# Kernel tuning notes

Measured on AMD Instinct MI355X. Metric: run time of the kernel, lower is better.

Reference implementation:

```python
import jax, jax.numpy as jnp
import numpy as np

N = 25000   # nodes of type 'window'
E = 200000  # edges per relation
H = 512     # hidden_channels
OUT = 250   # out_channels
L = 4       # num_layers
R = 3       # relations: near, close, sim


def setup_inputs() -> dict:
    key = jax.random.key(0)
    ks = jax.random.split(key, 8)
    s = 1.0 / np.sqrt(H).astype(np.float32)
    x = jax.random.normal(ks[0], (N, H), jnp.float32)
    W_pre = jax.random.normal(ks[1], (H, H), jnp.float32) * s
    W_post = jax.random.normal(ks[2], (H, H), jnp.float32) * s
    Wl = jax.random.normal(ks[3], (L, R, H, H), jnp.float32) * s   # SAGEConv lin_l (neighbors)
    Wr = jax.random.normal(ks[4], (L, R, H, H), jnp.float32) * s   # SAGEConv lin_r (root)
    bl = jnp.zeros((L, R, H), jnp.float32)                         # lin_l bias
    W_out = jax.random.normal(ks[5], (H, OUT), jnp.float32) * s
    b_out = jnp.zeros((OUT,), jnp.float32)
    edges = jax.random.randint(ks[6], (R, 2, E), 0, N, jnp.int32)  # [rel, (src,dst), E]
    return dict(x=x, W_pre=W_pre, W_post=W_post, Wl=Wl, Wr=Wr, bl=bl,
                W_out=W_out, b_out=b_out, edges=edges)


def _leaky(v):
    return jnp.where(v >= 0, v, 0.2 * v)


def reference(x, W_pre, W_post, Wl, Wr, bl, W_out, b_out, edges):
    # pretransform + post_transform: leaky(leaky(x @ Wpre) @ Wpost)
    h = _leaky(_leaky(x @ W_pre) @ W_post)

    # per-relation destination in-degree (constant across layers)
    inv_deg = []
    for r in range(R):
        cnt = jax.ops.segment_sum(jnp.ones((E,), h.dtype), edges[r, 1], num_segments=N)
        inv_deg.append(1.0 / jnp.maximum(cnt, 1.0))  # [N]

    for l in range(L):
        acc = jnp.zeros_like(h)
        for r in range(R):
            src, dst = edges[r, 0], edges[r, 1]
            # mean aggregation of neighbor features over destinations
            agg = jax.ops.segment_sum(h[src], dst, num_segments=N) * inv_deg[r][:, None]
            # SAGEConv: lin_l(agg) + lin_r(x_root)
            acc = acc + (agg @ Wl[l, r] + bl[l, r] + h @ Wr[l, r])
        # HeteroConv aggr='mean' across relations, then LeakyReLU(0.2)
        h = _leaky(acc / R)

    return h @ W_out + b_out
```

## Files before the change

kernel.cpp:

```cpp
#include <hip/hip_runtime.h>

#define N_ 25000
#define E_ 200000
#define H_ 512
#define OUT_ 250
#define WSZ (H_ * H_)

typedef unsigned short u16;
typedef unsigned int u32;
typedef __bf16 bf16x8 __attribute__((ext_vector_type(8)));
typedef float f32x4 __attribute__((ext_vector_type(4)));

__device__ __forceinline__ u16 f2b(float f) {
  union { float f; u32 u; } c; c.f = f;
  u32 r = c.u + 0x7FFFu + ((c.u >> 16) & 1u);
  return (u16)(r >> 16);
}
__device__ __forceinline__ void async16(const void* g, void* l) {
  __builtin_amdgcn_global_load_lds((__attribute__((address_space(1))) void*)g,
                                   (__attribute__((address_space(3))) void*)l, 16, 0, 0);
}

__global__ void conv_x(const float* __restrict__ x, u16* __restrict__ xb, int n4) {
  int i = blockIdx.x * 256 + threadIdx.x;
  if (i >= n4) return;
  const float4 v = *(const float4*)(x + (size_t)i * 4);
  ushort4 o;
  o.x = f2b(v.x); o.y = f2b(v.y); o.z = f2b(v.z); o.w = f2b(v.w);
  *(ushort4*)(xb + (size_t)i * 4) = o;
}

__global__ void prep_wt(const float* __restrict__ Wpre, const float* __restrict__ Wpost,
                        const float* __restrict__ Wl, const float* __restrict__ Wr,
                        u16* __restrict__ WT) {
  __shared__ u16 tile[32][33];
  const int id = blockIdx.z;
  const int tx = blockIdx.x, ty = blockIdx.y;
  const int x = threadIdx.x, y = threadIdx.y;
  const float* src = nullptr;
  bool sum3 = false;
  if (id == 0) src = Wpre;
  else if (id == 1) src = Wpost;
  else {
    int li = (id - 2) >> 2, ri = (id - 2) & 3;
    if (ri < 3) src = Wl + (size_t)(li * 3 + ri) * WSZ;
    else { sum3 = true; src = Wr + (size_t)(li * 3) * WSZ; }
  }
#pragma unroll
  for (int i = 0; i < 4; ++i) {
    int row = ty * 32 + y + i * 8;
    int col = tx * 32 + x;
    float f = src[(size_t)row * 512 + col];
    if (sum3) f += src[WSZ + (size_t)row * 512 + col] + src[2 * WSZ + (size_t)row * 512 + col];
    tile[y + i * 8][x] = f2b(f);
  }
  __syncthreads();
#pragma unroll
  for (int i = 0; i < 4; ++i) {
    WT[(size_t)id * WSZ + (tx * 32 + y + i * 8) * 512 + ty * 32 + x] = tile[x][y + i * 8];
  }
}

__global__ void prep_wout(const float* __restrict__ Wout, u16* __restrict__ WoutT) {
  __shared__ u16 tile[32][33];
  const int tx = blockIdx.x, ty = blockIdx.y;
  const int x = threadIdx.x, y = threadIdx.y;
#pragma unroll
  for (int i = 0; i < 4; ++i) {
    int row = ty * 32 + y + i * 8;
    int col = tx * 32 + x;
    tile[y + i * 8][x] = (col < OUT_) ? f2b(Wout[(size_t)row * OUT_ + col]) : (u16)0;
  }
  __syncthreads();
#pragma unroll
  for (int i = 0; i < 4; ++i) {
    WoutT[(tx * 32 + y + i * 8) * 512 + ty * 32 + x] = tile[x][y + i * 8];
  }
}

__global__ void prep_bias(const float* __restrict__ bl, const float* __restrict__ bout,
                          float* __restrict__ blSum, float* __restrict__ bOutF) {
  int t = threadIdx.x;
  for (int l = 0; l < 4; ++l)
    blSum[l * 512 + t] = bl[(l * 3 + 0) * 512 + t] + bl[(l * 3 + 1) * 512 + t] +
                         bl[(l * 3 + 2) * 512 + t];
  if (t < 256) bOutF[t] = (t < OUT_) ? bout[t] : 0.0f;
}

__global__ void hist_kernel(const int* __restrict__ edges, int* __restrict__ counts) {
  int idx = blockIdx.x * 256 + threadIdx.x;
  if (idx >= 3 * E_) return;
  int r = idx / E_, e = idx - r * E_;
  int dst = edges[r * 2 * E_ + E_ + e];
  atomicAdd(&counts[r * N_ + dst], 1);
}

__global__ __launch_bounds__(1024) void scan_kernel(const int* __restrict__ counts,
                                                    int* __restrict__ rowptr,
                                                    int* __restrict__ cursor,
                                                    float* __restrict__ invdeg) {
  const int r = blockIdx.x;
  const int* cnt = counts + r * N_;
  int* rp = rowptr + r * (N_ + 1);
  int* cur = cursor + r * N_;
  __shared__ int wsum[2][16];
  const int tid = threadIdx.x;
  const int wv = tid >> 6, lane = tid & 63;
  int roff = 0;
  int par = 0;
  for (int base = 0; base < N_; base += 1024, par ^= 1) {
    int v = (base + tid < N_) ? cnt[base + tid] : 0;
    int inc = v;
#pragma unroll
    for (int d = 1; d < 64; d <<= 1) {
      int t = __shfl_up(inc, d, 64);
      if (lane >= d) inc += t;
    }
    if (lane == 63) wsum[par][wv] = inc;
    __syncthreads();
    if (tid < 16) {
      int s = wsum[par][tid];
#pragma unroll
      for (int d = 1; d < 16; d <<= 1) {
        int t = __shfl_up(s, d, 64);
        if (tid >= d) s += t;
      }
      wsum[par][tid] = s;
    }
    __syncthreads();
    int woff = (wv == 0) ? 0 : wsum[par][wv - 1];
    int excl = roff + woff + inc - v;
    if (base + tid < N_) {
      rp[base + tid] = excl; cur[base + tid] = excl;
      invdeg[r * N_ + base + tid] = 1.0f / fmaxf((float)v, 1.0f);
    }
    roff += wsum[par][15];
  }
  if (tid == 0) rp[N_] = roff;
}

__global__ void scatter_kernel(const int* __restrict__ edges, int* __restrict__ cursor,
                               int* __restrict__ colidx) {
  int idx = blockIdx.x * 256 + threadIdx.x;
  if (idx >= 3 * E_) return;
  int r = idx / E_, e = idx - r * E_;
  int src = edges[r * 2 * E_ + e];
  int dst = edges[r * 2 * E_ + E_ + e];
  int pos = atomicAdd(&cursor[r * N_ + dst], 1);
  colidx[r * E_ + pos] = src;
}

__device__ __forceinline__ void acc8(float* acc, uint4 u) {
  union { u32 u; float f; } c;
  c.u = u.x << 16;          acc[0] += c.f;
  c.u = u.x & 0xffff0000u;  acc[1] += c.f;
  c.u = u.y << 16;          acc[2] += c.f;
  c.u = u.y & 0xffff0000u;  acc[3] += c.f;
  c.u = u.z << 16;          acc[4] += c.f;
  c.u = u.z & 0xffff0000u;  acc[5] += c.f;
  c.u = u.w << 16;          acc[6] += c.f;
  c.u = u.w & 0xffff0000u;  acc[7] += c.f;
}

__global__ __launch_bounds__(256) void agg_kernel(const u16* __restrict__ h,
                                                  const int* __restrict__ rowptr,
                                                  const int* __restrict__ colidx,
                                                  const float* __restrict__ invdeg,
                                                  u16* __restrict__ agg) {
  const int chunk = blockIdx.x & 7;
  const int nb = blockIdx.x >> 3;
  const int r = blockIdx.y;
  const int wv = threadIdx.x >> 6;
  const int lane = threadIdx.x & 63;
  const int grp = lane >> 3, sub = lane & 7;
  const int node = nb * 32 + wv * 8 + grp;
  if (node >= N_) return;
  const int* rp = rowptr + r * (N_ + 1);
  const int* ci = colidx + r * E_;
  const u16* hb = h + chunk * 64 + sub * 8;
  const int s = rp[node], e = rp[node + 1];
  float acc[8] = {0.f, 0.f, 0.f, 0.f, 0.f, 0.f, 0.f, 0.f};
  int p = s;
  if (p < e) {
    int src = ci[p];
    uint4 u = *(const uint4*)(hb + (size_t)src * 512);
    for (++p; p < e; ++p) {
      int src2 = ci[p];
      uint4 u2 = *(const uint4*)(hb + (size_t)src2 * 512);
      acc8(acc, u);
      u = u2;
    }
    acc8(acc, u);
  }
  const float sc = invdeg[r * N_ + node];
  uint4 o;
  o.x = (u32)f2b(acc[0] * sc) | ((u32)f2b(acc[1] * sc) << 16);
  o.y = (u32)f2b(acc[2] * sc) | ((u32)f2b(acc[3] * sc) << 16);
  o.z = (u32)f2b(acc[4] * sc) | ((u32)f2b(acc[5] * sc) << 16);
  o.w = (u32)f2b(acc[6] * sc) | ((u32)f2b(acc[7] * sc) << 16);
  *(uint4*)(agg + ((size_t)r * N_ + node) * 512 + chunk * 64 + sub * 8) = o;
}

#define BM 128
#define BN 128
#define BK 64
__global__ __launch_bounds__(256, 4) void gemm_mfma(
    const u16* __restrict__ A0, const u16* __restrict__ A1,
    const u16* __restrict__ A2, const u16* __restrict__ A3,
    const u16* __restrict__ Bt, const float* __restrict__ bias,
    u16* __restrict__ C, float* __restrict__ Cf,
    int M, int G, int ldc, int Nreal, float scale, int leaky) {
  __shared__ __align__(16) u16 As[BM * BK];
  __shared__ __align__(16) u16 Bs[BN * BK];
  const int tid = threadIdx.x;
  const int lane = tid & 63;
  const int w = tid >> 6;

  const int gx = gridDim.x;
  const int lin = blockIdx.y * gx + blockIdx.x;
  const int gsz = gx * 8;
  const int grp = lin / gsz;
  const int l = lin - grp * gsz;
  const int rem = (int)gridDim.y - grp * 8;
  int by, bx;
  if (rem >= 8) { by = grp * 8 + (l & 7); bx = l >> 3; }
  else          { by = grp * 8 + l % rem; bx = l / rem; }
  const int row0 = by * BM;
  const int col0 = bx * BN;

  int aOff[4], bOff[4], lOff[4];
#pragma unroll
  for (int i = 0; i < 4; ++i) {
    const int idx = i * 256 + tid;
    const int arow = idx >> 3;
    const int c = (idx & 7) ^ (arow & 7);
    int grow = row0 + arow; if (grow >= M) grow = M - 1;
    aOff[i] = grow * 512 + c * 8;
    bOff[i] = (col0 + arow) * 512 + c * 8;
    lOff[i] = idx * 16;
  }

  const int lm = lane & 15;
  const int lk = lane >> 4;
  const int x0 = ((lk ^ (lane & 7)) << 3);
  const int x1 = (((4 + lk) ^ (lane & 7)) << 3);
  const int wm = (w >> 1) * 64;
  const int wn = (w & 1) * 64;
  int aRow[4], bRow[4];
#pragma unroll
  for (int i = 0; i < 4; ++i) {
    aRow[i] = (wm + i * 16 + lm) * BK;
    bRow[i] = (wn + i * 16 + lm) * BK;
  }

  f32x4 acc[4][4] = {};

  for (int g = 0; g < G; ++g) {
    const u16* Ag = (g == 0) ? A0 : (g == 1) ? A1 : (g == 2) ? A2 : A3;
    const u16* Bg = Bt + ((size_t)g << 18);
#pragma unroll
    for (int ki = 0; ki < 8; ++ki) {
      const u16* Ab = Ag + ki * 64;
      const u16* Bb = Bg + ki * 64;
#pragma unroll
      for (int i = 0; i < 4; ++i) {
        async16(Ab + aOff[i], (char*)As + lOff[i]);
        async16(Bb + bOff[i], (char*)Bs + lOff[i]);
      }
      __syncthreads();
      {
        bf16x8 af[4], bfr[4];
#pragma unroll
        for (int i = 0; i < 4; ++i) {
          af[i]  = *(const bf16x8*)((const char*)As + ((aRow[i] + x0) << 1));
          bfr[i] = *(const bf16x8*)((const char*)Bs + ((bRow[i] + x0) << 1));
        }
#pragma unroll
        for (int i = 0; i < 4; ++i)
#pragma unroll
          for (int j = 0; j < 4; ++j)
            acc[i][j] = __builtin_amdgcn_mfma_f32_16x16x32_bf16(af[i], bfr[j], acc[i][j], 0, 0, 0);
#pragma unroll
        for (int i = 0; i < 4; ++i) {
          af[i]  = *(const bf16x8*)((const char*)As + ((aRow[i] + x1) << 1));
          bfr[i] = *(const bf16x8*)((const char*)Bs + ((bRow[i] + x1) << 1));
        }
#pragma unroll
        for (int i = 0; i < 4; ++i)
#pragma unroll
          for (int j = 0; j < 4; ++j)
            acc[i][j] = __builtin_amdgcn_mfma_f32_16x16x32_bf16(af[i], bfr[j], acc[i][j], 0, 0, 0);
      }
      __syncthreads();
    }
  }

  const int crow_base = row0 + wm + (lk << 2);
  const int ccol_base = col0 + wn + lm;
#pragma unroll
  for (int i = 0; i < 4; ++i) {
#pragma unroll
    for (int j = 0; j < 4; ++j) {
      const int ccol = ccol_base + j * 16;
      const float badd = bias ? bias[ccol] : 0.0f;
#pragma unroll
      for (int rg = 0; rg < 4; ++rg) {
        const int crow = crow_base + i * 16 + rg;
        if (crow < M && ccol < Nreal) {
          float v = (acc[i][j][rg] + badd) * scale;
          if (leaky) v = (v >= 0.0f) ? v : 0.2f * v;
          if (Cf) Cf[(size_t)crow * ldc + ccol] = v;
          else    C[(size_t)crow * ldc + ccol] = f2b(v);
        }
      }
    }
  }
}

extern "C" void kernel_launch(void* const* d_in, const int* in_sizes, int n_in,
                              void* d_out, int out_size, void* d_ws, size_t ws_size,
                              hipStream_t stream) {
  const float* x     = (const float*)d_in[0];
  const float* Wpre  = (const float*)d_in[1];
  const float* Wpost = (const float*)d_in[2];
  const float* Wl    = (const float*)d_in[3];
  const float* Wr    = (const float*)d_in[4];
  const float* bl    = (const float*)d_in[5];
  const float* Wout  = (const float*)d_in[6];
  const float* bout  = (const float*)d_in[7];
  const int*   edges = (const int*)d_in[8];
  float* out = (float*)d_out;

  char* p = (char*)d_ws;
  auto alloc = [&](size_t b) { void* q = (void*)p; p += (b + 255) & ~(size_t)255; return q; };
  u16*   WT     = (u16*)alloc((size_t)18 * WSZ * 2);
  u16*   WoutT  = (u16*)alloc((size_t)256 * 512 * 2);
  float* blSum  = (float*)alloc(4 * 512 * 4);
  float* bOutF  = (float*)alloc(256 * 4);
  u16*   hA     = (u16*)alloc((size_t)N_ * 512 * 2);
  u16*   hB     = (u16*)alloc((size_t)N_ * 512 * 2);
  u16*   aggb   = (u16*)alloc((size_t)3 * N_ * 512 * 2);
  int*   counts = (int*)alloc(3 * N_ * 4);
  float* invdeg = (float*)alloc(3 * N_ * 4);
  int*   rowptr = (int*)alloc(3 * (N_ + 1) * 4);
  int*   cursor = (int*)alloc(3 * N_ * 4);
  int*   colidx = (int*)alloc((size_t)3 * E_ * 4);
  u16*   xb     = aggb;

  hipMemsetAsync(counts, 0, 3 * N_ * 4, stream);
  conv_x<<<(N_ * 512 / 4 + 255) / 256, 256, 0, stream>>>(x, xb, N_ * 512 / 4);
  prep_wt<<<dim3(16, 16, 18), dim3(32, 8), 0, stream>>>(Wpre, Wpost, Wl, Wr, WT);
  prep_wout<<<dim3(8, 16), dim3(32, 8), 0, stream>>>(Wout, WoutT);
  prep_bias<<<1, 512, 0, stream>>>(bl, bout, blSum, bOutF);
  hist_kernel<<<(3 * E_ + 255) / 256, 256, 0, stream>>>(edges, counts);
  scan_kernel<<<3, 1024, 0, stream>>>(counts, rowptr, cursor, invdeg);
  scatter_kernel<<<(3 * E_ + 255) / 256, 256, 0, stream>>>(edges, cursor, colidx);

  const dim3 blk(256);
  const dim3 g512(512 / BN, (N_ + BM - 1) / BM);
  const dim3 gagg(((N_ + 31) / 32) * 8, 3);
  gemm_mfma<<<g512, blk, 0, stream>>>(xb, xb, xb, xb, WT, nullptr, hA, nullptr,
                                      N_, 1, 512, 512, 1.0f, 1);
  gemm_mfma<<<g512, blk, 0, stream>>>(hA, hA, hA, hA, WT + WSZ, nullptr, hB, nullptr,
                                      N_, 1, 512, 512, 1.0f, 1);

  u16* hc = hB; u16* hn = hA;
  for (int l = 0; l < 4; ++l) {
    agg_kernel<<<gagg, blk, 0, stream>>>(hc, rowptr, colidx, invdeg, aggb);
    gemm_mfma<<<g512, blk, 0, stream>>>(aggb, aggb + (size_t)N_ * 512, aggb + (size_t)2 * N_ * 512, hc,
                                        WT + (size_t)(2 + 4 * l) * WSZ, blSum + l * 512, hn, nullptr,
                                        N_, 4, 512, 512, 1.0f / 3.0f, 1);
    u16* t = hc; hc = hn; hn = t;
  }
  const dim3 gout(256 / BN, (N_ + BM - 1) / BM);
  gemm_mfma<<<gout, blk, 0, stream>>>(hc, hc, hc, hc, WoutT, bOutF, nullptr, out,
                                      N_, 1, OUT_, OUT_, 1.0f, 0);
}
```

Measured before the change: 847.8 us.

## Fuse prep kernels, unroll aggregation gathers, and stage GEMM output through LDS

Merges the x conversion with the degree histogram, and merges the weight, output-weight and bias preparation into one kernel, cutting launch count. The neighbor aggregation loop now issues four independent row gathers per iteration to raise memory-level parallelism. The bf16 GEMM epilogue writes tiles to a padded shared buffer and then stores 16-byte coalesced rows instead of scattered 2-byte stores. This enlarges shared memory per block (128x136 bf16), which could lower occupancy.

```diff
diff --git a/kernel.cpp b/kernel.cpp
--- a/kernel.cpp
+++ b/kernel.cpp
@@ -21,22 +21,57 @@
                                    (__attribute__((address_space(3))) void*)l, 16, 0, 0);
 }
 
-__global__ void conv_x(const float* __restrict__ x, u16* __restrict__ xb, int n4) {
-  int i = blockIdx.x * 256 + threadIdx.x;
-  if (i >= n4) return;
-  const float4 v = *(const float4*)(x + (size_t)i * 4);
-  ushort4 o;
-  o.x = f2b(v.x); o.y = f2b(v.y); o.z = f2b(v.z); o.w = f2b(v.w);
-  *(ushort4*)(xb + (size_t)i * 4) = o;
-}
-
-__global__ void prep_wt(const float* __restrict__ Wpre, const float* __restrict__ Wpost,
-                        const float* __restrict__ Wl, const float* __restrict__ Wr,
-                        u16* __restrict__ WT) {
+__global__ void conv_hist(const float* __restrict__ x, u16* __restrict__ xb,
+                          const int* __restrict__ edges, int* __restrict__ counts) {
+  const int i = blockIdx.x * 256 + threadIdx.x;
+  if (i < 3 * E_) {
+    int r = i / E_, e = i - r * E_;
+    int dst = edges[r * 2 * E_ + E_ + e];
+    atomicAdd(&counts[r * N_ + dst], 1);
+  }
+  if (i < N_ * 512 / 4) {
+    const float4 v = *(const float4*)(x + (size_t)i * 4);
+    ushort4 o;
+    o.x = f2b(v.x); o.y = f2b(v.y); o.z = f2b(v.z); o.w = f2b(v.w);
+    *(ushort4*)(xb + (size_t)i * 4) = o;
+  }
+}
+
+__global__ void prep_all(const float* __restrict__ Wpre, const float* __restrict__ Wpost,
+                         const float* __restrict__ Wl, const float* __restrict__ Wr,
+                         const float* __restrict__ Wout, const float* __restrict__ bl,
+                         const float* __restrict__ bout,
+                         u16* __restrict__ WT, u16* __restrict__ WoutT,
+                         float* __restrict__ blSum, float* __restrict__ bOutF) {
   __shared__ u16 tile[32][33];
   const int id = blockIdx.z;
   const int tx = blockIdx.x, ty = blockIdx.y;
   const int x = threadIdx.x, y = threadIdx.y;
+  if (id == 19) {
+    if (tx || ty) return;
+    const int t = y * 32 + x;
+    for (int t0 = t; t0 < 512; t0 += 256) {
+      for (int l = 0; l < 4; ++l)
+        blSum[l * 512 + t0] = bl[(l * 3 + 0) * 512 + t0] + bl[(l * 3 + 1) * 512 + t0] +
+                              bl[(l * 3 + 2) * 512 + t0];
+    }
+    if (t < 256) bOutF[t] = (t < OUT_) ? bout[t] : 0.0f;
+    return;
+  }
+  if (id == 18) {
+    if (tx >= 8) return;
+#pragma unroll
+    for (int i = 0; i < 4; ++i) {
+      int row = ty * 32 + y + i * 8;
+      int col = tx * 32 + x;
+      tile[y + i * 8][x] = (col < OUT_) ? f2b(Wout[(size_t)row * OUT_ + col]) : (u16)0;
+    }
+    __syncthreads();
+#pragma unroll
+    for (int i = 0; i < 4; ++i)
+      WoutT[(tx * 32 + y + i * 8) * 512 + ty * 32 + x] = tile[x][y + i * 8];
+    return;
+  }
   const float* src = nullptr;
   bool sum3 = false;
   if (id == 0) src = Wpre;
@@ -56,43 +91,8 @@
   }
   __syncthreads();
 #pragma unroll
-  for (int i = 0; i < 4; ++i) {
+  for (int i = 0; i < 4; ++i)
     WT[(size_t)id * WSZ + (tx * 32 + y + i * 8) * 512 + ty * 32 + x] = tile[x][y + i * 8];
-  }
-}
-
-__global__ void prep_wout(const float* __restrict__ Wout, u16* __restrict__ WoutT) {
-  __shared__ u16 tile[32][33];
-  const int tx = blockIdx.x, ty = blockIdx.y;
-  const int x = threadIdx.x, y = threadIdx.y;
-#pragma unroll
-  for (int i = 0; i < 4; ++i) {
-    int row = ty * 32 + y + i * 8;
-    int col = tx * 32 + x;
-    tile[y + i * 8][x] = (col < OUT_) ? f2b(Wout[(size_t)row * OUT_ + col]) : (u16)0;
-  }
-  __syncthreads();
-#pragma unroll
-  for (int i = 0; i < 4; ++i) {
-    WoutT[(tx * 32 + y + i * 8) * 512 + ty * 32 + x] = tile[x][y + i * 8];
-  }
-}
-
-__global__ void prep_bias(const float* __restrict__ bl, const float* __restrict__ bout,
-                          float* __restrict__ blSum, float* __restrict__ bOutF) {
-  int t = threadIdx.x;
-  for (int l = 0; l < 4; ++l)
-    blSum[l * 512 + t] = bl[(l * 3 + 0) * 512 + t] + bl[(l * 3 + 1) * 512 + t] +
-                         bl[(l * 3 + 2) * 512 + t];
-  if (t < 256) bOutF[t] = (t < OUT_) ? bout[t] : 0.0f;
-}
-
-__global__ void hist_kernel(const int* __restrict__ edges, int* __restrict__ counts) {
-  int idx = blockIdx.x * 256 + threadIdx.x;
-  if (idx >= 3 * E_) return;
-  int r = idx / E_, e = idx - r * E_;
-  int dst = edges[r * 2 * E_ + E_ + e];
-  atomicAdd(&counts[r * N_ + dst], 1);
 }
 
 __global__ __launch_bounds__(1024) void scan_kernel(const int* __restrict__ counts,
@@ -181,17 +181,15 @@
   const int s = rp[node], e = rp[node + 1];
   float acc[8] = {0.f, 0.f, 0.f, 0.f, 0.f, 0.f, 0.f, 0.f};
   int p = s;
-  if (p < e) {
-    int src = ci[p];
-    uint4 u = *(const uint4*)(hb + (size_t)src * 512);
-    for (++p; p < e; ++p) {
-      int src2 = ci[p];
-      uint4 u2 = *(const uint4*)(hb + (size_t)src2 * 512);
-      acc8(acc, u);
-      u = u2;
-    }
-    acc8(acc, u);
-  }
+  for (; p + 4 <= e; p += 4) {
+    int s0 = ci[p], s1 = ci[p + 1], s2 = ci[p + 2], s3 = ci[p + 3];
+    uint4 u0 = *(const uint4*)(hb + (size_t)s0 * 512);
+    uint4 u1 = *(const uint4*)(hb + (size_t)s1 * 512);
+    uint4 u2 = *(const uint4*)(hb + (size_t)s2 * 512);
+    uint4 u3 = *(const uint4*)(hb + (size_t)s3 * 512);
+    acc8(acc, u0); acc8(acc, u1); acc8(acc, u2); acc8(acc, u3);
+  }
+  for (; p < e; ++p) acc8(acc, *(const uint4*)(hb + (size_t)ci[p] * 512));
   const float sc = invdeg[r * N_ + node];
   uint4 o;
   o.x = (u32)f2b(acc[0] * sc) | ((u32)f2b(acc[1] * sc) << 16);
@@ -204,14 +202,16 @@
 #define BM 128
 #define BN 128
 #define BK 64
+#define CSTRIDE 136
 __global__ __launch_bounds__(256, 4) void gemm_mfma(
     const u16* __restrict__ A0, const u16* __restrict__ A1,
     const u16* __restrict__ A2, const u16* __restrict__ A3,
     const u16* __restrict__ Bt, const float* __restrict__ bias,
     u16* __restrict__ C, float* __restrict__ Cf,
     int M, int G, int ldc, int Nreal, float scale, int leaky) {
-  __shared__ __align__(16) u16 As[BM * BK];
-  __shared__ __align__(16) u16 Bs[BN * BK];
+  __shared__ __align__(16) u16 shmem[BM * CSTRIDE];
+  u16* As = shmem;
+  u16* Bs = shmem + BM * BK;
   const int tid = threadIdx.x;
   const int lane = tid & 63;
   const int w = tid >> 6;
@@ -295,23 +295,56 @@
     }
   }
 
-  const int crow_base = row0 + wm + (lk << 2);
-  const int ccol_base = col0 + wn + lm;
-#pragma unroll
-  for (int i = 0; i < 4; ++i) {
-#pragma unroll
-    for (int j = 0; j < 4; ++j) {
-      const int ccol = ccol_base + j * 16;
-      const float badd = bias ? bias[ccol] : 0.0f;
-#pragma unroll
-      for (int rg = 0; rg < 4; ++rg) {
-        const int crow = crow_base + i * 16 + rg;
-        if (crow < M && ccol < Nreal) {
+  if (Cf) {
+    const int crow_base = row0 + wm + (lk << 2);
+    const int ccol_base = col0 + wn + lm;
+#pragma unroll
+    for (int i = 0; i < 4; ++i) {
+#pragma unroll
+      for (int j = 0; j < 4; ++j) {
+        const int ccol = ccol_base + j * 16;
+        const float badd = bias ? bias[ccol] : 0.0f;
+#pragma unroll
+        for (int rg = 0; rg < 4; ++rg) {
+          const int crow = crow_base + i * 16 + rg;
+          if (crow < M && ccol < Nreal) {
+            float v = (acc[i][j][rg] + badd) * scale;
+            if (leaky) v = (v >= 0.0f) ? v : 0.2f * v;
+            Cf[(size_t)crow * ldc + ccol] = v;
+          }
+        }
+      }
+    }
+    return;
+  }
+  {
+    const int lrow_base = wm + (lk << 2);
+    const int lcol_base = wn + lm;
+#pragma unroll
+    for (int i = 0; i < 4; ++i) {
+#pragma unroll
+      for (int j = 0; j < 4; ++j) {
+        const int lcol = lcol_base + j * 16;
+        const float badd = bias ? bias[col0 + lcol] : 0.0f;
+#pragma unroll
+        for (int rg = 0; rg < 4; ++rg) {
+          const int lrow = lrow_base + i * 16 + rg;
           float v = (acc[i][j][rg] + badd) * scale;
           if (leaky) v = (v >= 0.0f) ? v : 0.2f * v;
-          if (Cf) Cf[(size_t)crow * ldc + ccol] = v;
-          else    C[(size_t)crow * ldc + ccol] = f2b(v);
+          shmem[lrow * CSTRIDE + lcol] = f2b(v);
         }
+      }
+    }
+    __syncthreads();
+    const int rr = tid >> 4;
+    const int c8 = (tid & 15) * 8;
+#pragma unroll
+    for (int pass = 0; pass < 8; ++pass) {
+      const int r = pass * 16 + rr;
+      const int crow = row0 + r;
+      if (crow < M) {
+        uint4 v = *(const uint4*)&shmem[r * CSTRIDE + c8];
+        *(uint4*)(C + (size_t)crow * ldc + col0 + c8) = v;
       }
     }
   }
@@ -348,11 +381,9 @@
   u16*   xb     = aggb;
 
   hipMemsetAsync(counts, 0, 3 * N_ * 4, stream);
-  conv_x<<<(N_ * 512 / 4 + 255) / 256, 256, 0, stream>>>(x, xb, N_ * 512 / 4);
-  prep_wt<<<dim3(16, 16, 18), dim3(32, 8), 0, stream>>>(Wpre, Wpost, Wl, Wr, WT);
-  prep_wout<<<dim3(8, 16), dim3(32, 8), 0, stream>>>(Wout, WoutT);
-  prep_bias<<<1, 512, 0, stream>>>(bl, bout, blSum, bOutF);
-  hist_kernel<<<(3 * E_ + 255) / 256, 256, 0, stream>>>(edges, counts);
+  conv_hist<<<(N_ * 512 / 4 + 255) / 256, 256, 0, stream>>>(x, xb, edges, counts);
+  prep_all<<<dim3(16, 16, 20), dim3(32, 8), 0, stream>>>(Wpre, Wpost, Wl, Wr, Wout, bl, bout,
+                                                          WT, WoutT, blSum, bOutF);
   scan_kernel<<<3, 1024, 0, stream>>>(counts, rowptr, cursor, invdeg);
   scatter_kernel<<<(3 * E_ + 255) / 256, 256, 0, stream>>>(edges, cursor, colidx);
 
```

Result: faster. 792.2 us (-6.5%).
